# Kernel optimization log

Hardware: AMD Instinct MI355X
Metric: run time of the kernel (lower is better)

The kernel has to match this reference:

```python
import jax, jax.numpy as jnp
import numpy as np

N_NODES = 100000
N_RELS = 1000
N_EDGES = 400000
DIM = 256  # even: split into real/imag halves


def setup_inputs() -> dict:
    key = jax.random.key(0)
    k1, k2, k3, k4, k5 = jax.random.split(key, 5)
    node_emb = jax.random.normal(k1, (N_NODES, DIM), dtype=jnp.float32)
    rel_emb = jax.random.normal(k2, (N_RELS, DIM), dtype=jnp.float32)
    src = jax.random.randint(k3, (N_EDGES,), 0, N_NODES, dtype=jnp.int64 if jax.config.jax_enable_x64 else jnp.int32).astype(jnp.int32)
    dst = jax.random.randint(k4, (N_EDGES,), 0, N_NODES).astype(jnp.int32)
    rel_id = jax.random.randint(k5, (N_EDGES,), 0, N_RELS).astype(jnp.int32)
    return {"node_emb": node_emb, "rel_emb": rel_emb, "src": src, "dst": dst, "rel_id": rel_id}


def reference(node_emb, rel_emb, src, dst, rel_id):
    h = node_emb[src]      # [E, D] gathered head embeddings
    t = node_emb[dst]      # [E, D] gathered tail embeddings
    r = rel_emb[rel_id]    # [E, D] gathered relation embeddings
    half = h.shape[-1] // 2
    rh, ih = h[:, :half], h[:, half:]
    rt, it = t[:, :half], t[:, half:]
    rr, ir = r[:, :half], r[:, half:]
    # ComplEx: Re(<h, r, conj(t)>)
    score = rh * rt * rr + ih * it * rr + rh * it * ir - ih * rt * ir
    return jnp.sum(score, axis=-1)  # [E]
```

## Files before the change

kernel.cpp:

```cpp
#include <hip/hip_runtime.h>
#include <hip/hip_fp16.h>
#include <string.h>

#define DIM 256

__global__ __launch_bounds__(256) void f32_to_f16_kernel(
    const float* __restrict__ in, int4* __restrict__ out, int n8)
{
    int i = blockIdx.x * blockDim.x + threadIdx.x;
    if (i >= n8) return;
    const float4* p = (const float4*)in + 2 * (size_t)i;
    float4 a = p[0];
    float4 b = p[1];
    __half2 h0 = __float22half2_rn(make_float2(a.x, a.y));
    __half2 h1 = __float22half2_rn(make_float2(a.z, a.w));
    __half2 h2 = __float22half2_rn(make_float2(b.x, b.y));
    __half2 h3 = __float22half2_rn(make_float2(b.z, b.w));
    int4 o;
    memcpy(&o.x, &h0, 4);
    memcpy(&o.y, &h1, 4);
    memcpy(&o.z, &h2, 4);
    memcpy(&o.w, &h3, 4);
    out[i] = o;
}

__global__ __launch_bounds__(256) void complex_score_f16_kernel(
    const __half* __restrict__ node,
    const __half* __restrict__ rel,
    const int* __restrict__ src,
    const int* __restrict__ dst,
    const int* __restrict__ rid,
    float* __restrict__ out,
    int n_edges)
{
    const int tid  = blockIdx.x * blockDim.x + threadIdx.x;
    const int edge = tid >> 5;
    const int lane = tid & 31;
    if (edge >= n_edges) return;

    const int s = src[edge];
    const int d = dst[edge];
    const int r = rid[edge];

    const int4* hp = (const int4*)(node + (size_t)s * DIM);
    const int4* tp = (const int4*)(node + (size_t)d * DIM);
    const int4* rp = (const int4*)(rel  + (size_t)r * DIM);

    int4 hv = hp[lane];
    int4 tv = tp[lane];
    int4 rv = rp[lane];

    int4 hq, tq;
    hq.x = __shfl_xor(hv.x, 16); hq.y = __shfl_xor(hv.y, 16);
    hq.z = __shfl_xor(hv.z, 16); hq.w = __shfl_xor(hv.w, 16);
    tq.x = __shfl_xor(tv.x, 16); tq.y = __shfl_xor(tv.y, 16);
    tq.z = __shfl_xor(tv.z, 16); tq.w = __shfl_xor(tv.w, 16);

    const bool hi = (lane & 16) != 0;
    float acc = 0.0f;

    #define UP(v, f2) { __half2 _h; memcpy(&_h, &(v), 4); f2 = __half22float2(_h); }
    #define TERM(c) { \
        float2 oh, ph, ot, pt, rr; \
        UP(hv.c, oh); UP(hq.c, ph); \
        UP(tv.c, ot); UP(tq.c, pt); \
        UP(rv.c, rr); \
        float tx = hi ? (ph.x * ot.x - oh.x * pt.x) : (oh.x * ot.x + ph.x * pt.x); \
        float ty = hi ? (ph.y * ot.y - oh.y * pt.y) : (oh.y * ot.y + ph.y * pt.y); \
        acc = fmaf(rr.x, tx, acc); \
        acc = fmaf(rr.y, ty, acc); }

    TERM(x) TERM(y) TERM(z) TERM(w)
    #undef TERM
    #undef UP

    #pragma unroll
    for (int off = 16; off > 0; off >>= 1)
        acc += __shfl_xor(acc, off);

    if (lane == 0)
        out[edge] = acc;
}

__global__ __launch_bounds__(256) void complex_score_f32_kernel(
    const float* __restrict__ node_emb,
    const float* __restrict__ rel_emb,
    const int* __restrict__ src,
    const int* __restrict__ dst,
    const int* __restrict__ rel_id,
    float* __restrict__ out,
    int n_edges)
{
    const int tid  = blockIdx.x * blockDim.x + threadIdx.x;
    const int edge = tid >> 5;
    const int lane = tid & 31;
    if (edge >= n_edges) return;

    const int s = src[edge];
    const int d = dst[edge];
    const int r = rel_id[edge];

    const float4* hp = (const float4*)(node_emb + (size_t)s * DIM);
    const float4* tp = (const float4*)(node_emb + (size_t)d * DIM);
    const float4* rp = (const float4*)(rel_emb  + (size_t)r * DIM);

    float4 rh = hp[lane];
    float4 ih = hp[lane + 32];
    float4 rt = tp[lane];
    float4 it = tp[lane + 32];
    float4 rr = rp[lane];
    float4 ir = rp[lane + 32];

    float a0 = rr.x * (rh.x * rt.x + ih.x * it.x) + ir.x * (rh.x * it.x - ih.x * rt.x);
    float a1 = rr.y * (rh.y * rt.y + ih.y * it.y) + ir.y * (rh.y * it.y - ih.y * rt.y);
    float a2 = rr.z * (rh.z * rt.z + ih.z * it.z) + ir.z * (rh.z * it.z - ih.z * rt.z);
    float a3 = rr.w * (rh.w * rt.w + ih.w * it.w) + ir.w * (rh.w * it.w - ih.w * rt.w);
    float acc = (a0 + a1) + (a2 + a3);

    #pragma unroll
    for (int off = 16; off > 0; off >>= 1)
        acc += __shfl_xor(acc, off, 32);

    if (lane == 0)
        out[edge] = acc;
}

extern "C" void kernel_launch(void* const* d_in, const int* in_sizes, int n_in,
                              void* d_out, int out_size, void* d_ws, size_t ws_size,
                              hipStream_t stream) {
    const float* node_emb = (const float*)d_in[0];
    const float* rel_emb  = (const float*)d_in[1];
    const int*   src      = (const int*)d_in[2];
    const int*   dst      = (const int*)d_in[3];
    const int*   rel_id   = (const int*)d_in[4];
    float* out = (float*)d_out;

    const int n_edges = in_sizes[2];
    const int n_nodes = in_sizes[0] / DIM;
    const int n_rels  = in_sizes[1] / DIM;

    const size_t f16_bytes = ((size_t)n_nodes + (size_t)n_rels) * DIM * 2;

    const int tpb = 256;
    const long long total_threads = (long long)n_edges * 32;
    const int score_blocks = (int)((total_threads + tpb - 1) / tpb);

    if (ws_size >= f16_bytes) {
        __half* node_f16 = (__half*)d_ws;
        __half* rel_f16  = node_f16 + (size_t)n_nodes * DIM;

        const int n8_node = n_nodes * DIM / 8;
        const int n8_rel  = n_rels  * DIM / 8;

        f32_to_f16_kernel<<<(n8_node + tpb - 1) / tpb, tpb, 0, stream>>>(
            node_emb, (int4*)node_f16, n8_node);
        f32_to_f16_kernel<<<(n8_rel + tpb - 1) / tpb, tpb, 0, stream>>>(
            rel_emb, (int4*)rel_f16, n8_rel);

        complex_score_f16_kernel<<<score_blocks, tpb, 0, stream>>>(
            node_f16, rel_f16, src, dst, rel_id, out, n_edges);
    } else {
        complex_score_f32_kernel<<<score_blocks, tpb, 0, stream>>>(
            node_emb, rel_emb, src, dst, rel_id, out, n_edges);
    }
}
```

Baseline: 226.0 us.

## Interleave real/imag halves in f16 copy and use fdot2 for ComplEx terms

Result: no change. 229.7 us (+1.7%).

```diff
diff --git a/kernel.cpp b/kernel.cpp
--- a/kernel.cpp
+++ b/kernel.cpp
@@ -4,27 +4,69 @@
 
 #define DIM 256
 
-__global__ __launch_bounds__(256) void f32_to_f16_kernel(
-    const float* __restrict__ in, int4* __restrict__ out, int n8)
+typedef __attribute__((ext_vector_type(2))) _Float16 half2v;
+
+#if defined(__has_builtin)
+#if __has_builtin(__builtin_amdgcn_fdot2)
+#define HAVE_FDOT2 1
+#endif
+#endif
+
+__global__ __launch_bounds__(256) void f32_to_f16i_kernel(
+    const float* __restrict__ in, int4* __restrict__ out, int nrows)
 {
     int i = blockIdx.x * blockDim.x + threadIdx.x;
-    if (i >= n8) return;
-    const float4* p = (const float4*)in + 2 * (size_t)i;
-    float4 a = p[0];
-    float4 b = p[1];
-    __half2 h0 = __float22half2_rn(make_float2(a.x, a.y));
-    __half2 h1 = __float22half2_rn(make_float2(a.z, a.w));
-    __half2 h2 = __float22half2_rn(make_float2(b.x, b.y));
-    __half2 h3 = __float22half2_rn(make_float2(b.z, b.w));
+    int row = i >> 5;
+    int q   = i & 31;
+    if (row >= nrows) return;
+
+    const float4* re = (const float4*)(in + (size_t)row * DIM) + q;
+    const float4* im = (const float4*)(in + (size_t)row * DIM + 128) + q;
+    float4 a = *re;
+    float4 b = *im;
+
+    __half2 p0 = __float22half2_rn(make_float2(a.x, b.x));
+    __half2 p1 = __float22half2_rn(make_float2(a.y, b.y));
+    __half2 p2 = __float22half2_rn(make_float2(a.z, b.z));
+    __half2 p3 = __float22half2_rn(make_float2(a.w, b.w));
+
     int4 o;
-    memcpy(&o.x, &h0, 4);
-    memcpy(&o.y, &h1, 4);
-    memcpy(&o.z, &h2, 4);
-    memcpy(&o.w, &h3, 4);
-    out[i] = o;
+    memcpy(&o.x, &p0, 4);
+    memcpy(&o.y, &p1, 4);
+    memcpy(&o.z, &p2, 4);
+    memcpy(&o.w, &p3, 4);
+    out[(size_t)row * 32 + q] = o;
 }
 
-__global__ __launch_bounds__(256) void complex_score_f16_kernel(
+__device__ __forceinline__ float pair_term(int h32, int t32, int r32, float acc)
+{
+    unsigned tu = (unsigned)t32;
+    unsigned tsw = (tu >> 16) | ((tu << 16) ^ 0x80000000u);
+
+    half2v h2, t2, r2, ts2;
+    memcpy(&h2, &h32, 4);
+    memcpy(&t2, &t32, 4);
+    memcpy(&r2, &r32, 4);
+    memcpy(&ts2, &tsw, 4);
+
+#ifdef HAVE_FDOT2
+    float u = __builtin_amdgcn_fdot2(r2, t2, 0.0f, false);
+    float v = __builtin_amdgcn_fdot2(r2, ts2, 0.0f, false);
+#else
+    float rr = (float)r2.x, ir = (float)r2.y;
+    float rt = (float)t2.x, it = (float)t2.y;
+    float u = rr * rt + ir * it;
+    float v = rr * it - ir * rt;
+    (void)ts2;
+#endif
+    float rh = (float)h2.x;
+    float ih = (float)h2.y;
+    acc = fmaf(rh, u, acc);
+    acc = fmaf(ih, v, acc);
+    return acc;
+}
+
+__global__ __launch_bounds__(256) void complex_score_f16i_kernel(
     const __half* __restrict__ node,
     const __half* __restrict__ rel,
     const int* __restrict__ src,
@@ -50,29 +92,11 @@
     int4 tv = tp[lane];
     int4 rv = rp[lane];
 
-    int4 hq, tq;
-    hq.x = __shfl_xor(hv.x, 16); hq.y = __shfl_xor(hv.y, 16);
-    hq.z = __shfl_xor(hv.z, 16); hq.w = __shfl_xor(hv.w, 16);
-    tq.x = __shfl_xor(tv.x, 16); tq.y = __shfl_xor(tv.y, 16);
-    tq.z = __shfl_xor(tv.z, 16); tq.w = __shfl_xor(tv.w, 16);
-
-    const bool hi = (lane & 16) != 0;
     float acc = 0.0f;
-
-    #define UP(v, f2) { __half2 _h; memcpy(&_h, &(v), 4); f2 = __half22float2(_h); }
-    #define TERM(c) { \
-        float2 oh, ph, ot, pt, rr; \
-        UP(hv.c, oh); UP(hq.c, ph); \
-        UP(tv.c, ot); UP(tq.c, pt); \
-        UP(rv.c, rr); \
-        float tx = hi ? (ph.x * ot.x - oh.x * pt.x) : (oh.x * ot.x + ph.x * pt.x); \
-        float ty = hi ? (ph.y * ot.y - oh.y * pt.y) : (oh.y * ot.y + ph.y * pt.y); \
-        acc = fmaf(rr.x, tx, acc); \
-        acc = fmaf(rr.y, ty, acc); }
-
-    TERM(x) TERM(y) TERM(z) TERM(w)
-    #undef TERM
-    #undef UP
+    acc = pair_term(hv.x, tv.x, rv.x, acc);
+    acc = pair_term(hv.y, tv.y, rv.y, acc);
+    acc = pair_term(hv.z, tv.z, rv.z, acc);
+    acc = pair_term(hv.w, tv.w, rv.w, acc);
 
     #pragma unroll
     for (int off = 16; off > 0; off >>= 1)
@@ -149,15 +173,15 @@
         __half* node_f16 = (__half*)d_ws;
         __half* rel_f16  = node_f16 + (size_t)n_nodes * DIM;
 
-        const int n8_node = n_nodes * DIM / 8;
-        const int n8_rel  = n_rels  * DIM / 8;
+        const int node_threads = n_nodes * 32;
+        const int rel_threads  = n_rels * 32;
 
-        f32_to_f16_kernel<<<(n8_node + tpb - 1) / tpb, tpb, 0, stream>>>(
-            node_emb, (int4*)node_f16, n8_node);
-        f32_to_f16_kernel<<<(n8_rel + tpb - 1) / tpb, tpb, 0, stream>>>(
-            rel_emb, (int4*)rel_f16, n8_rel);
+        f32_to_f16i_kernel<<<(node_threads + tpb - 1) / tpb, tpb, 0, stream>>>(
+            node_emb, (int4*)node_f16, n_nodes);
+        f32_to_f16i_kernel<<<(rel_threads + tpb - 1) / tpb, tpb, 0, stream>>>(
+            rel_emb, (int4*)rel_f16, n_rels);
 
-        complex_score_f16_kernel<<<score_blocks, tpb, 0, stream>>>(
+        complex_score_f16i_kernel<<<score_blocks, tpb, 0, stream>>>(
             node_f16, rel_f16, src, dst, rel_id, out, n_edges);
     } else {
         complex_score_f32_kernel<<<score_blocks, tpb, 0, stream>>>(
```
